# Performance work log

Measured on AMD Instinct MI355X. Metric: run time of the kernel, lower is better.

The kernel has to match this reference:

```python
import jax, jax.numpy as jnp
import numpy as np

K = 3          # kernel_size
PAD = 1        # padding for offset conv and deform conv
UPS = 2        # ConvTranspose2d stride
EPS = 1e-5     # BatchNorm eps


def _conv2d(x, w, b, pad):
    y = jax.lax.conv_general_dilated(x, w, (1, 1), [(pad, pad), (pad, pad)],
                                     dimension_numbers=('NCHW', 'OIHW', 'NCHW'))
    return y + b[None, :, None, None]


def _deform_conv(x, offsets, w, b):
    # torchvision DeformConv2d semantics, stride=1, pad=1, dilation=1
    B, C, H, W = x.shape
    KK = K * K
    off = offsets.reshape(B, KK, 2, H, W)  # [:, kk, 0]=dy, [:, kk, 1]=dx
    ki, kj = jnp.meshgrid(jnp.arange(K), jnp.arange(K), indexing='ij')
    py = (jnp.arange(H) - PAD)[None, None, :, None] + ki.ravel()[None, :, None, None] + off[:, :, 0]
    px = (jnp.arange(W) - PAD)[None, None, None, :] + kj.ravel()[None, :, None, None] + off[:, :, 1]
    y0f = jnp.floor(py); x0f = jnp.floor(px)
    ly = py - y0f; lx = px - x0f
    y0 = y0f.astype(jnp.int32); x0 = x0f.astype(jnp.int32)
    xf = x.reshape(B, C, H * W)

    def corner(yy, xx, wgt):
        valid = (yy >= 0) & (yy < H) & (xx >= 0) & (xx < W)
        idx = jnp.clip(yy, 0, H - 1) * W + jnp.clip(xx, 0, W - 1)      # [B,KK,H,W]
        v = jax.vmap(lambda f, i: f[:, i])(xf, idx)                     # [B,C,KK,H,W]
        return v * (wgt * valid)[:, None]

    s = (corner(y0, x0, (1 - ly) * (1 - lx)) + corner(y0, x0 + 1, (1 - ly) * lx)
         + corner(y0 + 1, x0, ly * (1 - lx)) + corner(y0 + 1, x0 + 1, ly * lx))
    out = jnp.einsum('bckhw,ock->bohw', s, w.reshape(w.shape[0], C, KK))
    return out + b[None, :, None, None]


def _conv_transpose(x, w, b):
    # torch ConvTranspose2d(stride=UPS, padding=0); torch weight is [C_in, C_out, K, K]
    wf = jnp.flip(jnp.transpose(w, (1, 0, 2, 3)), (2, 3))
    y = jax.lax.conv_general_dilated(x, wf, (1, 1), [(K - 1, K - 1)] * 2,
                                     lhs_dilation=(UPS, UPS),
                                     dimension_numbers=('NCHW', 'OIHW', 'NCHW'))
    return y + b[None, :, None, None]


def setup_inputs() -> dict:
    key = jax.random.key(0)
    ks = jax.random.split(key, 8)
    B, Cin, Cout, H, W = 16, 64, 128, 64, 64
    s = 0.05
    return {
        'x': jax.random.normal(ks[0], (B, Cin, H, W), jnp.float32),
        'w_off': jax.random.normal(ks[1], (2 * K * K, Cin, K, K), jnp.float32) * s,
        'b_off': jax.random.normal(ks[2], (2 * K * K,), jnp.float32) * s,
        'w_def': jax.random.normal(ks[3], (Cout, Cin, K, K), jnp.float32) * s,
        'b_def': jax.random.normal(ks[4], (Cout,), jnp.float32) * s,
        'w_up': jax.random.normal(ks[5], (Cout, Cout, K, K), jnp.float32) * s,
        'b_up': jax.random.normal(ks[6], (Cout,), jnp.float32) * s,
        'gamma': jnp.ones((Cout,), jnp.float32),
        'beta': jnp.zeros((Cout,), jnp.float32),
    }


def reference(x, w_off, b_off, w_def, b_def, w_up, b_up, gamma, beta):
    offsets = _conv2d(x, w_off, b_off, PAD)
    feats = _deform_conv(x, offsets, w_def, b_def)
    y = _conv_transpose(feats, w_up, b_up)
    # BatchNorm2d (training mode, biased batch stats) + ReLU
    mu = jnp.mean(y, axis=(0, 2, 3), keepdims=True)
    var = jnp.var(y, axis=(0, 2, 3), keepdims=True)
    yn = (y - mu) * jax.lax.rsqrt(var + EPS)
    yn = yn * gamma[None, :, None, None] + beta[None, :, None, None]
    return jax.nn.relu(yn)
```

## Files before the change

### kernel.cpp

```cpp
#include <hip/hip_runtime.h>
#include <math.h>

#define PADC 1
#define CIN  64
#define COUT 128
#define IH   64
#define IW   64
#define NB   16
#define OYX  129
#define NOFF 18
#define SPO  (OYX * OYX)
#define BNEPS 1e-5f
#define NBLK_CT (NB * OYX)

typedef __attribute__((ext_vector_type(8))) short bf16x8;
typedef __attribute__((ext_vector_type(4))) float f32x4;

static __device__ __forceinline__ unsigned short f2bf(float f) {
    unsigned int b = __float_as_uint(f);
    unsigned int r = (b + 0x7FFFu + ((b >> 16) & 1u)) >> 16;
    return (unsigned short)r;
}
static __device__ __forceinline__ float bf2f(unsigned short u) {
    return __uint_as_float((unsigned int)u << 16);
}

__global__ void k_prep(const float* __restrict__ w_def, const float* __restrict__ w_up,
                       const float* __restrict__ w_off,
                       unsigned short* __restrict__ WDF, unsigned short* __restrict__ WB,
                       unsigned short* __restrict__ WOF)
{
    int idx = blockIdx.x * 256 + threadIdx.x;
    if (idx < 73728) {
        const int j = idx & 7;
        const int n = (idx >> 3) & 127;
        const int g = idx >> 10;
        const int kg = g & 3, ks = (g >> 2) & 1, kk = g >> 3;
        const int c = ks * 32 + kg * 8 + j;
        WDF[idx] = f2bf(w_def[(n * CIN + c) * 9 + kk]);
    }
    const int i2 = idx - 73728;
    if (i2 >= 0 && i2 < 147456) {
        const int j = i2 & 7;
        const int n = (i2 >> 3) & 127;
        int ky, kx, ci;
        if (i2 < 65536) {
            const int k = (i2 >> 10) * 8 + j;
            ky = (k >> 8) ? 0 : 2;
            kx = ((k >> 7) & 1) ? 0 : 2;
            ci = k & 127;
        } else if (i2 < 98304) {
            const int k = ((i2 - 65536) >> 10) * 8 + j;
            ky = 1;
            kx = (k >> 7) ? 0 : 2;
            ci = k & 127;
        } else if (i2 < 131072) {
            const int k = ((i2 - 98304) >> 10) * 8 + j;
            ky = (k >> 7) ? 0 : 2;
            kx = 1;
            ci = k & 127;
        } else {
            const int k = ((i2 - 131072) >> 10) * 8 + j;
            ky = 1; kx = 1;
            ci = k & 127;
        }
        WB[i2] = f2bf(w_up[((ci * COUT + n) * 3 + ky) * 3 + kx]);
    }
    const int i3 = idx - 221184;
    if (i3 >= 0 && i3 < 18432) {
        const int j = i3 & 7;
        const int n = (i3 >> 3) & 31;
        const int g = i3 >> 8;
        const int kg = g & 3, s = g >> 2;
        const int c  = (s & 1) * 32 + kg * 8 + j;
        const int kk = s >> 1;
        const int ki = kk / 3, kj = kk - 3 * ki;
        WOF[i3] = (n < NOFF) ? f2bf(w_off[((n * CIN + c) * 3 + ki) * 3 + kj]) : (unsigned short)0;
    }
}

__global__ __launch_bounds__(256) void k_xt(const float* __restrict__ x, unsigned short* __restrict__ xt)
{
    __shared__ unsigned short t[64][66];
    const int tid = threadIdx.x;
    const int h = blockIdx.x & 63, b = blockIdx.x >> 6;
    const int w = tid & 63, cq = tid >> 6;
    #pragma unroll
    for (int p = 0; p < 16; ++p) {
        const int c = p * 4 + cq;
        t[w][c] = f2bf(x[((size_t)((b * 64 + c) * 64) + h) * 64 + w]);
    }
    __syncthreads();
    const int w2 = tid >> 2, q = tid & 3;
    unsigned int pk[8];
    #pragma unroll
    for (int m = 0; m < 8; ++m)
        pk[m] = (unsigned int)t[w2][q * 16 + 2 * m] | ((unsigned int)t[w2][q * 16 + 2 * m + 1] << 16);
    uint4* dst = (uint4*)(xt + ((size_t)((b * 64 + h) * 64) + w2) * 64 + q * 16);
    dst[0] = uint4{pk[0], pk[1], pk[2], pk[3]};
    dst[1] = uint4{pk[4], pk[5], pk[6], pk[7]};
}

__global__ __launch_bounds__(64, 4) void k_offset_mfma(
    const unsigned short* __restrict__ xt, const unsigned short* __restrict__ WOF,
    const float* __restrict__ b_off, float* __restrict__ offs)
{
    const int l  = threadIdx.x;
    const int ml = l & 15;
    const int kg = l >> 4;
    const int q  = blockIdx.x & 3;
    const int h  = (blockIdx.x >> 2) & 63;
    const int b  = blockIdx.x >> 8;
    const int w  = q * 16 + ml;
    const unsigned short* xb = xt + (size_t)b * (IH * IW * CIN);

    const f32x4 fz = {0.f, 0.f, 0.f, 0.f};
    f32x4 acc0 = fz, acc1 = fz;

    #pragma unroll 1
    for (int s = 0; s < 18; ++s) {
        const int kk = s >> 1;
        const int ki = kk / 3, kj = kk - 3 * ki;
        const int c0 = (s & 1) * 32 + kg * 8;
        const int yy = h - PADC + ki;
        const int xx = w - PADC + kj;
        const bf16x8 b0 = *(const bf16x8*)(WOF + (size_t)(((s * 4 + kg) * 32 + ml) * 8));
        const bf16x8 b1 = *(const bf16x8*)(WOF + (size_t)(((s * 4 + kg) * 32 + 16 + ml) * 8));
        bf16x8 a = {0, 0, 0, 0, 0, 0, 0, 0};
        if (yy >= 0 && yy < IH && xx >= 0 && xx < IW)
            a = *(const bf16x8*)(xb + (size_t)((yy * IW + xx) * CIN) + c0);
        acc0 = __builtin_amdgcn_mfma_f32_16x16x32_bf16(a, b0, acc0, 0, 0, 0);
        acc1 = __builtin_amdgcn_mfma_f32_16x16x32_bf16(a, b1, acc1, 0, 0, 0);
    }
    #pragma unroll
    for (int nt = 0; nt < 2; ++nt) {
        const int oc = nt * 16 + ml;
        if (oc < NOFF) {
            const float bias = b_off[oc];
            const f32x4 av = nt ? acc1 : acc0;
            #pragma unroll
            for (int j = 0; j < 4; ++j) {
                const int wd = q * 16 + kg * 4 + j;
                offs[((size_t)(b * NOFF + oc) * IH + h) * IW + wd] = av[j] + bias;
            }
        }
    }
}

__global__ __launch_bounds__(64, 4) void k_deform_mfma(
    const unsigned short* __restrict__ xt, const float* __restrict__ offs,
    const unsigned short* __restrict__ WDF, const float* __restrict__ b_def,
    unsigned short* __restrict__ feats_bf)
{
    const int l  = threadIdx.x;
    const int ml = l & 15;
    const int kg = l >> 4;
    const int q  = blockIdx.x & 3;
    const int h  = (blockIdx.x >> 2) & 63;
    const int b  = blockIdx.x >> 8;
    const int w  = q * 16 + ml;

    const unsigned short* xb = xt + (size_t)b * (IH * IW * CIN);

    const f32x4 fz = {0.f, 0.f, 0.f, 0.f};
    f32x4 acc[8];
    #pragma unroll
    for (int nt = 0; nt < 8; ++nt) acc[nt] = fz;

    #pragma unroll 1
    for (int kk = 0; kk < 9; ++kk) {
        const int ki = kk / 3, kj = kk - 3 * ki;
        const float dy = offs[((b * NOFF + 2 * kk) * IH + h) * IW + w];
        const float dx = offs[((b * NOFF + 2 * kk + 1) * IH + h) * IW + w];
        const float py = (float)(h - PADC + ki) + dy;
        const float px = (float)(w - PADC + kj) + dx;
        const float y0f = floorf(py), x0f = floorf(px);
        const float ly = py - y0f, lx = px - x0f;
        const int y0 = (int)y0f, x0 = (int)x0f;
        const float wy[2] = {1.f - ly, ly};
        const float wx[2] = {1.f - lx, lx};
        int   cidx[4];
        float cwgt[4];
        #pragma unroll
        for (int cy = 0; cy < 2; ++cy)
            #pragma unroll
            for (int cx = 0; cx < 2; ++cx) {
                const int yy = y0 + cy, xx = x0 + cx;
                const bool v = (yy >= 0) & (yy < IH) & (xx >= 0) & (xx < IW);
                cidx[cy * 2 + cx] = v ? ((yy * IW + xx) * CIN) : 0;
                cwgt[cy * 2 + cx] = v ? (wy[cy] * wx[cx]) : 0.f;
            }
        #pragma unroll
        for (int ks = 0; ks < 2; ++ks) {
            const int c0 = ks * 32 + kg * 8;
            uint4 cv[4];
            #pragma unroll
            for (int cp = 0; cp < 4; ++cp)
                cv[cp] = *(const uint4*)(xb + cidx[cp] + c0);
            bf16x8 bfr[8];
            #pragma unroll
            for (int nt = 0; nt < 8; ++nt)
                bfr[nt] = *(const bf16x8*)(WDF + ((size_t)((kk * 8 + ks * 4 + kg) * 128) + nt * 16 + ml) * 8);
            float sf[8] = {0.f, 0.f, 0.f, 0.f, 0.f, 0.f, 0.f, 0.f};
            #pragma unroll
            for (int cp = 0; cp < 4; ++cp) {
                const float wg = cwgt[cp];
                const unsigned int u0 = cv[cp].x, u1 = cv[cp].y, u2 = cv[cp].z, u3 = cv[cp].w;
                sf[0] += wg * __uint_as_float(u0 << 16);
                sf[1] += wg * __uint_as_float(u0 & 0xFFFF0000u);
                sf[2] += wg * __uint_as_float(u1 << 16);
                sf[3] += wg * __uint_as_float(u1 & 0xFFFF0000u);
                sf[4] += wg * __uint_as_float(u2 << 16);
                sf[5] += wg * __uint_as_float(u2 & 0xFFFF0000u);
                sf[6] += wg * __uint_as_float(u3 << 16);
                sf[7] += wg * __uint_as_float(u3 & 0xFFFF0000u);
            }
            union { unsigned short us[8]; bf16x8 v; } pa;
            #pragma unroll
            for (int j = 0; j < 8; ++j) pa.us[j] = f2bf(sf[j]);
            #pragma unroll
            for (int nt = 0; nt < 8; ++nt)
                acc[nt] = __builtin_amdgcn_mfma_f32_16x16x32_bf16(pa.v, bfr[nt], acc[nt], 0, 0, 0);
        }
    }
    #pragma unroll
    for (int nt = 0; nt < 8; ++nt) {
        const int o = nt * 16 + ml;
        const float bias = b_def[o];
        #pragma unroll
        for (int j = 0; j < 4; ++j) {
            const int wd = q * 16 + kg * 4 + j;
            feats_bf[((size_t)((b * IH + h) * IW) + wd) * COUT + o] = f2bf(acc[nt][j] + bias);
        }
    }
}

__global__ __launch_bounds__(256) void k_convT_mfma(
    const unsigned short* __restrict__ feats_bf, const unsigned short* __restrict__ WB,
    unsigned short* __restrict__ y_bf, float* __restrict__ partials)
{
    __shared__ __align__(16) char smem[34048];

    const int tid = threadIdx.x;
    const int l   = tid & 63;
    const int wv  = tid >> 6;
    const int ml  = l & 15;
    const int kg  = l >> 4;
    const int blk = blockIdx.x;
    const int oy  = blk % OYX;
    const int b   = blk / OYX;
    const int py  = oy & 1;
    const int ty  = oy >> 1;

    const int nrow = py ? 1 : 2;
    int iys[2];
    if (py == 0) { iys[0] = ty - 1; iys[1] = (ty <= 63) ? ty : -1; }
    else         { iys[0] = ty;     iys[1] = -1; }

    for (int r = 0; r < nrow; ++r) {
        char* dstbase = smem + r * 16896;
        const int iy = iys[r];
        if (iy < 0 || iy > 63) {
            for (int i = tid; i < 1056; i += 256)
                *(uint4*)(dstbase + i * 16) = uint4{0, 0, 0, 0};
        } else {
            const unsigned short* src = feats_bf + (size_t)(b * IH + iy) * (IW * COUT);
            for (int i = tid; i < 1024; i += 256) {
                const uint4 v = *(const uint4*)(src + i * 8);
                const int G = 16 + i;
                const int phys = G ^ ((G >> 4) & 7);
                *(uint4*)(dstbase + phys * 16) = v;
            }
            if (tid < 32) {
                const int G = (tid < 16) ? tid : (1024 + tid);
                const int phys = G ^ ((G >> 4) & 7);
                *(uint4*)(dstbase + phys * 16) = uint4{0, 0, 0, 0};
            }
        }
    }
    __syncthreads();

    const f32x4 fz = {0.f, 0.f, 0.f, 0.f};
    f32x4 acc0[5][2], acc1[4][2];
    #pragma unroll
    for (int m = 0; m < 5; ++m) { acc0[m][0] = fz; acc0[m][1] = fz; }
    #pragma unroll
    for (int m = 0; m < 4; ++m) { acc1[m][0] = fz; acc1[m][1] = fz; }

    const int n0   = wv * 32;
    const int nK0  = py ? 8 : 16;
    const int nK1  = py ? 4 : 8;
    const unsigned short* segG0 = WB + (py ? 65536 : 0);
    const unsigned short* segG1 = WB + (py ? 131072 : 98304);

    for (int ks = 0; ks < nK0; ++ks) {
        const int kk   = ks * 32 + kg * 8;
        const int slot = kk >> 8;
        const int kb   = (kk & 255) >> 3;
        const bf16x8 b0 = *(const bf16x8*)(segG0 + ((ks * 4 + kg) * 128 + n0 + ml) * 8);
        const bf16x8 b1 = *(const bf16x8*)(segG0 + ((ks * 4 + kg) * 128 + n0 + 16 + ml) * 8);
        #pragma unroll
        for (int mt = 0; mt < 5; ++mt) {
            int tx = mt * 16 + ml; if (tx > 64) tx = 64;
            const int G = tx * 16 + kb;
            const int phys = G ^ ((G >> 4) & 7);
            const bf16x8 a = *(const bf16x8*)(smem + slot * 16896 + phys * 16);
            acc0[mt][0] = __builtin_amdgcn_mfma_f32_16x16x32_bf16(a, b0, acc0[mt][0], 0, 0, 0);
            acc0[mt][1] = __builtin_amdgcn_mfma_f32_16x16x32_bf16(a, b1, acc0[mt][1], 0, 0, 0);
        }
    }
    for (int ks = 0; ks < nK1; ++ks) {
        const int kk   = ks * 32 + kg * 8;
        const int slot = kk >> 7;
        const int kb   = (kk & 127) >> 3;
        const bf16x8 b0 = *(const bf16x8*)(segG1 + ((ks * 4 + kg) * 128 + n0 + ml) * 8);
        const bf16x8 b1 = *(const bf16x8*)(segG1 + ((ks * 4 + kg) * 128 + n0 + 16 + ml) * 8);
        #pragma unroll
        for (int mt = 0; mt < 4; ++mt) {
            const int tx = mt * 16 + ml;
            const int G = 16 + tx * 16 + kb;
            const int phys = G ^ ((G >> 4) & 7);
            const bf16x8 a = *(const bf16x8*)(smem + slot * 16896 + phys * 16);
            acc1[mt][0] = __builtin_amdgcn_mfma_f32_16x16x32_bf16(a, b0, acc1[mt][0], 0, 0, 0);
            acc1[mt][1] = __builtin_amdgcn_mfma_f32_16x16x32_bf16(a, b1, acc1[mt][1], 0, 0, 0);
        }
    }

    __syncthreads();
    float* slab = (float*)smem + wv * 2128;
    const int rrow = kg * 4;
    #pragma unroll
    for (int nt = 0; nt < 2; ++nt) {
        #pragma unroll
        for (int mt = 0; mt < 5; ++mt) {
            #pragma unroll
            for (int j = 0; j < 4; ++j) {
                const int tx = mt * 16 + rrow + j;
                if (tx <= 64) slab[ml * 133 + 2 * tx] = acc0[mt][nt][j];
            }
        }
        #pragma unroll
        for (int mt = 0; mt < 4; ++mt) {
            #pragma unroll
            for (int j = 0; j < 4; ++j) {
                const int tx = mt * 16 + rrow + j;
                slab[ml * 133 + 2 * tx + 1] = acc1[mt][nt][j];
            }
        }
        __syncthreads();
        #pragma unroll
        for (int r2 = 0; r2 < 16; ++r2) {
            const int co = n0 + nt * 16 + r2;
            unsigned short* drow = y_bf + ((size_t)(b * COUT + co) * OYX + oy) * OYX;
            drow[l]      = f2bf(slab[r2 * 133 + l]);
            drow[64 + l] = f2bf(slab[r2 * 133 + 64 + l]);
            if (l == 0) drow[128] = f2bf(slab[r2 * 133 + 128]);
        }
        {
            const int r = ml;
            const int g = kg;
            float s = 0.f, q = 0.f;
            #pragma unroll
            for (int t = 0; t < 33; ++t) {
                const int cx = g + 4 * t;
                if (cx < 129) {
                    const float v = slab[r * 133 + cx];
                    s += v; q += v * v;
                }
            }
            s += __shfl_xor(s, 16, 64); q += __shfl_xor(q, 16, 64);
            s += __shfl_xor(s, 32, 64); q += __shfl_xor(q, 32, 64);
            if (kg == 0) {
                float* pp = partials + ((size_t)blk * COUT + n0 + nt * 16 + ml) * 2;
                pp[0] = s; pp[1] = q;
            }
        }
        __syncthreads();
    }
}

__global__ __launch_bounds__(256) void k_bn_final(const float* __restrict__ partials,
                                                  float* __restrict__ stats)
{
    const int c = blockIdx.x;
    const int tid = threadIdx.x;
    float s = 0.f, q = 0.f;
    for (int i = tid; i < NBLK_CT; i += 256) {
        const float* pp = partials + ((size_t)i * COUT + c) * 2;
        s += pp[0]; q += pp[1];
    }
    __shared__ float rs[256], rq[256];
    rs[tid] = s; rq[tid] = q;
    __syncthreads();
    for (int off = 128; off > 0; off >>= 1) {
        if (tid < off) { rs[tid] += rs[tid + off]; rq[tid] += rq[tid + off]; }
        __syncthreads();
    }
    if (tid == 0) {
        const float n = (float)(NB * SPO);
        const float mean = rs[0] / n;
        const float var  = rq[0] / n - mean * mean;
        stats[c] = mean;
        stats[COUT + c] = rsqrtf(var + BNEPS);
    }
}

__global__ void k_bn_apply(const unsigned short* __restrict__ y_bf, float* __restrict__ y,
                           const float* __restrict__ stats,
                           const float* __restrict__ gamma, const float* __restrict__ beta)
{
    const int i = blockIdx.x * 256 + threadIdx.x;
    const int c = (i / SPO) & (COUT - 1);
    const float mean = stats[c], rstd = stats[COUT + c];
    float v = bf2f(y_bf[i]);
    v = (v - mean) * rstd * gamma[c] + beta[c];
    y[i] = fmaxf(v, 0.f);
}

extern "C" void kernel_launch(void* const* d_in, const int* in_sizes, int n_in,
                              void* d_out, int out_size, void* d_ws, size_t ws_size,
                              hipStream_t stream)
{
    const float* x     = (const float*)d_in[0];
    const float* w_off = (const float*)d_in[1];
    const float* b_off = (const float*)d_in[2];
    const float* w_def = (const float*)d_in[3];
    const float* b_def = (const float*)d_in[4];
    const float* w_up  = (const float*)d_in[5];
    const float* b_up  = (const float*)d_in[6];  (void)b_up;
    const float* gamma = (const float*)d_in[7];
    const float* beta  = (const float*)d_in[8];
    float* y = (float*)d_out;

    float* ws       = (float*)d_ws;
    float* offs     = ws;
    float* stats    = offs + 1179648;
    float* partials = stats + 256;
    unsigned short* xt       = (unsigned short*)(partials + 528384);
    unsigned short* WDF      = xt + 4194304;
    unsigned short* feats_bf = WDF + 73728;
    unsigned short* WB       = feats_bf + 8388608;
    unsigned short* WOF      = WB + 147456;
    unsigned short* y_bf     = WOF + 18432;

    k_prep        <<<dim3(936),    dim3(256), 0, stream>>>(w_def, w_up, w_off, WDF, WB, WOF);
    k_xt          <<<dim3(1024),   dim3(256), 0, stream>>>(x, xt);
    k_offset_mfma <<<dim3(4096),   dim3(64),  0, stream>>>(xt, WOF, b_off, offs);
    k_deform_mfma <<<dim3(4096),   dim3(64),  0, stream>>>(xt, offs, WDF, b_def, feats_bf);
    k_convT_mfma  <<<dim3(NBLK_CT),dim3(256), 0, stream>>>(feats_bf, WB, y_bf, partials);
    k_bn_final    <<<dim3(128),    dim3(256), 0, stream>>>(partials, stats);
    k_bn_apply    <<<dim3(133128), dim3(256), 0, stream>>>(y_bf, y, stats, gamma, beta);
}
```

Measured before the change: 198.4 us.

## Merge conv-transpose output row pairs per block and vectorize BN apply

Each conv-transpose block now computes both output rows (even and odd parity) that share the same two staged input rows. This halves the number of blocks and the redundant feature-row loads into shared memory. Results are packed as interleaved bf16 pairs and written straight from registers into a row-padded (136-wide) intermediate, replacing the shared-memory slab, its barriers and the separate stats pass; BN partial sums are now accumulated in registers. The BN apply kernel reads 8 bf16 values per thread with a uint4 load from the padded layout. In exchange there is less block-level parallelism, a serial loop over the two parities, and a larger padded intermediate buffer in workspace.

```diff
diff --git a/kernel.cpp b/kernel.cpp
--- a/kernel.cpp
+++ b/kernel.cpp
@@ -8,10 +8,11 @@
 #define IW   64
 #define NB   16
 #define OYX  129
+#define OXP  136
 #define NOFF 18
 #define SPO  (OYX * OYX)
 #define BNEPS 1e-5f
-#define NBLK_CT (NB * OYX)
+#define NBLK_CT (NB * 65)
 
 typedef __attribute__((ext_vector_type(8))) short bf16x8;
 typedef __attribute__((ext_vector_type(4))) float f32x4;
@@ -239,7 +240,7 @@
     const unsigned short* __restrict__ feats_bf, const unsigned short* __restrict__ WB,
     unsigned short* __restrict__ y_bf, float* __restrict__ partials)
 {
-    __shared__ __align__(16) char smem[34048];
+    __shared__ __align__(16) char smem[33792];
 
     const int tid = threadIdx.x;
     const int l   = tid & 63;
@@ -247,19 +248,12 @@
     const int ml  = l & 15;
     const int kg  = l >> 4;
     const int blk = blockIdx.x;
-    const int oy  = blk % OYX;
-    const int b   = blk / OYX;
-    const int py  = oy & 1;
-    const int ty  = oy >> 1;
-
-    const int nrow = py ? 1 : 2;
-    int iys[2];
-    if (py == 0) { iys[0] = ty - 1; iys[1] = (ty <= 63) ? ty : -1; }
-    else         { iys[0] = ty;     iys[1] = -1; }
-
-    for (int r = 0; r < nrow; ++r) {
+    const int t   = blk % 65;
+    const int b   = blk / 65;
+
+    for (int r = 0; r < 2; ++r) {
         char* dstbase = smem + r * 16896;
-        const int iy = iys[r];
+        const int iy = t - 1 + r;
         if (iy < 0 || iy > 63) {
             for (int i = tid; i < 1056; i += 256)
                 *(uint4*)(dstbase + i * 16) = uint4{0, 0, 0, 0};
@@ -280,102 +274,93 @@
     }
     __syncthreads();
 
+    const int n0 = wv * 32;
     const f32x4 fz = {0.f, 0.f, 0.f, 0.f};
-    f32x4 acc0[5][2], acc1[4][2];
-    #pragma unroll
-    for (int m = 0; m < 5; ++m) { acc0[m][0] = fz; acc0[m][1] = fz; }
-    #pragma unroll
-    for (int m = 0; m < 4; ++m) { acc1[m][0] = fz; acc1[m][1] = fz; }
-
-    const int n0   = wv * 32;
-    const int nK0  = py ? 8 : 16;
-    const int nK1  = py ? 4 : 8;
-    const unsigned short* segG0 = WB + (py ? 65536 : 0);
-    const unsigned short* segG1 = WB + (py ? 131072 : 98304);
-
-    for (int ks = 0; ks < nK0; ++ks) {
-        const int kk   = ks * 32 + kg * 8;
-        const int slot = kk >> 8;
-        const int kb   = (kk & 255) >> 3;
-        const bf16x8 b0 = *(const bf16x8*)(segG0 + ((ks * 4 + kg) * 128 + n0 + ml) * 8);
-        const bf16x8 b1 = *(const bf16x8*)(segG0 + ((ks * 4 + kg) * 128 + n0 + 16 + ml) * 8);
-        #pragma unroll
-        for (int mt = 0; mt < 5; ++mt) {
-            int tx = mt * 16 + ml; if (tx > 64) tx = 64;
-            const int G = tx * 16 + kb;
-            const int phys = G ^ ((G >> 4) & 7);
-            const bf16x8 a = *(const bf16x8*)(smem + slot * 16896 + phys * 16);
-            acc0[mt][0] = __builtin_amdgcn_mfma_f32_16x16x32_bf16(a, b0, acc0[mt][0], 0, 0, 0);
-            acc0[mt][1] = __builtin_amdgcn_mfma_f32_16x16x32_bf16(a, b1, acc0[mt][1], 0, 0, 0);
-        }
-    }
-    for (int ks = 0; ks < nK1; ++ks) {
-        const int kk   = ks * 32 + kg * 8;
-        const int slot = kk >> 7;
-        const int kb   = (kk & 127) >> 3;
-        const bf16x8 b0 = *(const bf16x8*)(segG1 + ((ks * 4 + kg) * 128 + n0 + ml) * 8);
-        const bf16x8 b1 = *(const bf16x8*)(segG1 + ((ks * 4 + kg) * 128 + n0 + 16 + ml) * 8);
-        #pragma unroll
-        for (int mt = 0; mt < 4; ++mt) {
-            const int tx = mt * 16 + ml;
-            const int G = 16 + tx * 16 + kb;
-            const int phys = G ^ ((G >> 4) & 7);
-            const bf16x8 a = *(const bf16x8*)(smem + slot * 16896 + phys * 16);
-            acc1[mt][0] = __builtin_amdgcn_mfma_f32_16x16x32_bf16(a, b0, acc1[mt][0], 0, 0, 0);
-            acc1[mt][1] = __builtin_amdgcn_mfma_f32_16x16x32_bf16(a, b1, acc1[mt][1], 0, 0, 0);
-        }
-    }
-
-    __syncthreads();
-    float* slab = (float*)smem + wv * 2128;
-    const int rrow = kg * 4;
+    float sacc[2] = {0.f, 0.f}, qacc[2] = {0.f, 0.f};
+
+    #pragma unroll 1
+    for (int p = 0; p < 2; ++p) {
+        if (p == 1 && t == 64) break;
+        const int oy = 2 * t + p;
+        const unsigned short* segG0 = WB + (p ? 65536 : 0);
+        const unsigned short* segG1 = WB + (p ? 131072 : 98304);
+        const int nK0 = p ? 8 : 16;
+        const int nK1 = p ? 4 : 8;
+
+        f32x4 acc0[5][2], acc1[4][2];
+        #pragma unroll
+        for (int m = 0; m < 5; ++m) { acc0[m][0] = fz; acc0[m][1] = fz; }
+        #pragma unroll
+        for (int m = 0; m < 4; ++m) { acc1[m][0] = fz; acc1[m][1] = fz; }
+
+        for (int ks = 0; ks < nK0; ++ks) {
+            const int kk   = ks * 32 + kg * 8;
+            const int slot = p ? 1 : (kk >> 8);
+            const int kb   = (kk & 255) >> 3;
+            const bf16x8 b0 = *(const bf16x8*)(segG0 + ((ks * 4 + kg) * 128 + n0 + ml) * 8);
+            const bf16x8 b1 = *(const bf16x8*)(segG0 + ((ks * 4 + kg) * 128 + n0 + 16 + ml) * 8);
+            #pragma unroll
+            for (int mt = 0; mt < 5; ++mt) {
+                int tx = mt * 16 + ml; if (tx > 64) tx = 64;
+                const int G = tx * 16 + kb;
+                const int phys = G ^ ((G >> 4) & 7);
+                const bf16x8 a = *(const bf16x8*)(smem + slot * 16896 + phys * 16);
+                acc0[mt][0] = __builtin_amdgcn_mfma_f32_16x16x32_bf16(a, b0, acc0[mt][0], 0, 0, 0);
+                acc0[mt][1] = __builtin_amdgcn_mfma_f32_16x16x32_bf16(a, b1, acc0[mt][1], 0, 0, 0);
+            }
+        }
+        for (int ks = 0; ks < nK1; ++ks) {
+            const int kk   = ks * 32 + kg * 8;
+            const int slot = p ? 1 : (kk >> 7);
+            const int kb   = (kk & 127) >> 3;
+            const bf16x8 b0 = *(const bf16x8*)(segG1 + ((ks * 4 + kg) * 128 + n0 + ml) * 8);
+            const bf16x8 b1 = *(const bf16x8*)(segG1 + ((ks * 4 + kg) * 128 + n0 + 16 + ml) * 8);
+            #pragma unroll
+            for (int mt = 0; mt < 4; ++mt) {
+                const int tx = mt * 16 + ml;
+                const int G = 16 + tx * 16 + kb;
+                const int phys = G ^ ((G >> 4) & 7);
+                const bf16x8 a = *(const bf16x8*)(smem + slot * 16896 + phys * 16);
+                acc1[mt][0] = __builtin_amdgcn_mfma_f32_16x16x32_bf16(a, b0, acc1[mt][0], 0, 0, 0);
+                acc1[mt][1] = __builtin_amdgcn_mfma_f32_16x16x32_bf16(a, b1, acc1[mt][1], 0, 0, 0);
+            }
+        }
+
+        #pragma unroll
+        for (int nt = 0; nt < 2; ++nt) {
+            const int co = n0 + nt * 16 + ml;
+            unsigned int* drow32 = (unsigned int*)(y_bf + ((size_t)(b * COUT + co) * OYX + oy) * OXP);
+            #pragma unroll
+            for (int mt = 0; mt < 4; ++mt) {
+                unsigned int pk[4];
+                #pragma unroll
+                for (int j = 0; j < 4; ++j) {
+                    const float ve = acc0[mt][nt][j];
+                    const float vo = acc1[mt][nt][j];
+                    pk[j] = (unsigned int)f2bf(ve) | ((unsigned int)f2bf(vo) << 16);
+                    sacc[nt] += ve + vo;
+                    qacc[nt] += ve * ve + vo * vo;
+                }
+                *(uint4*)(drow32 + mt * 16 + kg * 4) = uint4{pk[0], pk[1], pk[2], pk[3]};
+            }
+            if (kg == 0) {
+                const float ve = acc0[4][nt][0];
+                drow32[64] = (unsigned int)f2bf(ve);
+                sacc[nt] += ve;
+                qacc[nt] += ve * ve;
+            }
+        }
+    }
+
     #pragma unroll
     for (int nt = 0; nt < 2; ++nt) {
-        #pragma unroll
-        for (int mt = 0; mt < 5; ++mt) {
-            #pragma unroll
-            for (int j = 0; j < 4; ++j) {
-                const int tx = mt * 16 + rrow + j;
-                if (tx <= 64) slab[ml * 133 + 2 * tx] = acc0[mt][nt][j];
-            }
-        }
-        #pragma unroll
-        for (int mt = 0; mt < 4; ++mt) {
-            #pragma unroll
-            for (int j = 0; j < 4; ++j) {
-                const int tx = mt * 16 + rrow + j;
-                slab[ml * 133 + 2 * tx + 1] = acc1[mt][nt][j];
-            }
-        }
-        __syncthreads();
-        #pragma unroll
-        for (int r2 = 0; r2 < 16; ++r2) {
-            const int co = n0 + nt * 16 + r2;
-            unsigned short* drow = y_bf + ((size_t)(b * COUT + co) * OYX + oy) * OYX;
-            drow[l]      = f2bf(slab[r2 * 133 + l]);
-            drow[64 + l] = f2bf(slab[r2 * 133 + 64 + l]);
-            if (l == 0) drow[128] = f2bf(slab[r2 * 133 + 128]);
-        }
-        {
-            const int r = ml;
-            const int g = kg;
-            float s = 0.f, q = 0.f;
-            #pragma unroll
-            for (int t = 0; t < 33; ++t) {
-                const int cx = g + 4 * t;
-                if (cx < 129) {
-                    const float v = slab[r * 133 + cx];
-                    s += v; q += v * v;
-                }
-            }
-            s += __shfl_xor(s, 16, 64); q += __shfl_xor(q, 16, 64);
-            s += __shfl_xor(s, 32, 64); q += __shfl_xor(q, 32, 64);
-            if (kg == 0) {
-                float* pp = partials + ((size_t)blk * COUT + n0 + nt * 16 + ml) * 2;
-                pp[0] = s; pp[1] = q;
-            }
-        }
-        __syncthreads();
+        float ss = sacc[nt], qq = qacc[nt];
+        ss += __shfl_xor(ss, 16, 64); qq += __shfl_xor(qq, 16, 64);
+        ss += __shfl_xor(ss, 32, 64); qq += __shfl_xor(qq, 32, 64);
+        if (kg == 0) {
+            float* pp = partials + ((size_t)blk * COUT + n0 + nt * 16 + ml) * 2;
+            pp[0] = ss; pp[1] = qq;
+        }
     }
 }
 
@@ -405,16 +390,32 @@
     }
 }
 
-__global__ void k_bn_apply(const unsigned short* __restrict__ y_bf, float* __restrict__ y,
-                           const float* __restrict__ stats,
-                           const float* __restrict__ gamma, const float* __restrict__ beta)
-{
-    const int i = blockIdx.x * 256 + threadIdx.x;
-    const int c = (i / SPO) & (COUT - 1);
-    const float mean = stats[c], rstd = stats[COUT + c];
-    float v = bf2f(y_bf[i]);
-    v = (v - mean) * rstd * gamma[c] + beta[c];
-    y[i] = fmaxf(v, 0.f);
+__global__ __launch_bounds__(256) void k_bn_apply(
+    const unsigned short* __restrict__ y_bf, float* __restrict__ y,
+    const float* __restrict__ stats,
+    const float* __restrict__ gamma, const float* __restrict__ beta)
+{
+    const int v = blockIdx.x * 256 + threadIdx.x;
+    const int rid = v / 17;
+    const int c   = v - rid * 17;
+    const int co  = (rid / OYX) & (COUT - 1);
+    const float mean = stats[co], rstd = stats[COUT + co];
+    const float ga = gamma[co], be = beta[co];
+    const int ox0 = c * 8;
+
+    const uint4 u = *(const uint4*)(y_bf + (size_t)rid * OXP + ox0);
+    const unsigned int uu[4] = {u.x, u.y, u.z, u.w};
+    float* dst = y + (size_t)rid * OYX + ox0;
+    const int nv = (c < 16) ? 8 : 1;
+    #pragma unroll
+    for (int m = 0; m < 4; ++m) {
+        float v0 = bf2f((unsigned short)(uu[m] & 0xFFFFu));
+        float v1 = bf2f((unsigned short)(uu[m] >> 16));
+        v0 = fmaxf((v0 - mean) * rstd * ga + be, 0.f);
+        v1 = fmaxf((v1 - mean) * rstd * ga + be, 0.f);
+        if (2 * m < nv)     dst[2 * m]     = v0;
+        if (2 * m + 1 < nv) dst[2 * m + 1] = v1;
+    }
 }
 
 extern "C" void kernel_launch(void* const* d_in, const int* in_sizes, int n_in,
@@ -449,5 +450,5 @@
     k_deform_mfma <<<dim3(4096),   dim3(64),  0, stream>>>(xt, offs, WDF, b_def, feats_bf);
     k_convT_mfma  <<<dim3(NBLK_CT),dim3(256), 0, stream>>>(feats_bf, WB, y_bf, partials);
     k_bn_final    <<<dim3(128),    dim3(256), 0, stream>>>(partials, stats);
-    k_bn_apply    <<<dim3(133128), dim3(256), 0, stream>>>(y_bf, y, stats, gamma, beta);
-}
+    k_bn_apply    <<<dim3(17544),  dim3(256), 0, stream>>>(y_bf, y, stats, gamma, beta);
+}
```

New measurement: 174.9 us. 11.9% less time.
